# Optimization experiments

Hardware: AMD Instinct MI355X
Metric: run time of the kernel (lower is better)

The kernel has to match this reference:

```python
import jax, jax.numpy as jnp
import numpy as np

BETA = 0.25
K = 1024   # num_codebook_vectors
D = 256    # latent_dim


def setup_inputs() -> dict:
    key = jax.random.key(0)
    k1, k2 = jax.random.split(key)
    z = jax.random.normal(k1, (16, D, 64, 64), dtype=jnp.float32)
    # embedding initialized uniform(-1/K, 1/K) as in the torch module
    emb = jax.random.uniform(k2, (K, D), dtype=jnp.float32, minval=-1.0 / K, maxval=1.0 / K)
    return {"z": z, "emb": emb}


def reference(z, emb):
    sg = jax.lax.stop_gradient
    # NCHW -> NHWC
    z_nhwc = jnp.transpose(z, (0, 2, 3, 1))            # [B,H,W,D]
    zf = z_nhwc.reshape(-1, D)                          # [N,D]
    # squared euclidean distances: ||z||^2 + ||e||^2 - 2 z e^T
    d = (jnp.sum(zf * zf, axis=1, keepdims=True)
         + jnp.sum(emb * emb, axis=1)
         - 2.0 * jnp.matmul(zf, emb.T))                 # [N,K]
    min_encoding_indices = jnp.argmin(d, axis=1)        # [N] int
    z_q = emb[min_encoding_indices].reshape(z_nhwc.shape)  # [B,H,W,D]
    # loss exactly as in source (first term is zero in value, faithful)
    loss = (jnp.mean((sg(z_nhwc) - z_nhwc) ** 2)
            + BETA * jnp.mean((z_q - sg(z_nhwc)) ** 2))
    # straight-through estimator
    z_q_st = z_nhwc + sg(z_q - z_nhwc)
    out = jnp.transpose(z_q_st, (0, 3, 1, 2))           # NHWC -> NCHW
    return out, min_encoding_indices, loss
```

## Files before the change

### kernel.cpp

```cpp
#include <hip/hip_runtime.h>

#define DD 256
#define KK 1024
#define HW 4096
#define NROWSZ 65536
#define OUT_Z 16777216
#define OUT_IDX OUT_Z
#define OUT_LOSS (OUT_Z + NROWSZ)

#define MARGIN 4.5e-4f

#define WS_ESQ   0
#define WS_EH    4096
#define WS_HLIST 528384
#define WS_HCNT  790528
#define WS_LSUM  790536
#define WS_EMBT  791552
#define WS_EHP   1840128

typedef _Float16 f16x8 __attribute__((ext_vector_type(8)));
typedef float f32x4 __attribute__((ext_vector_type(4)));
union U16x8 { uint4 u; f16x8 h; };
typedef unsigned long long u64;

static __device__ __forceinline__ u64 umin64(u64 a, u64 b) { return a < b ? a : b; }
static __device__ __forceinline__ unsigned pk16(float a, float b) {
    _Float16 ha = (_Float16)a, hb = (_Float16)b;
    return (unsigned)__builtin_bit_cast(unsigned short, ha)
         | ((unsigned)__builtin_bit_cast(unsigned short, hb) << 16);
}

__global__ void vq_prep(const float* __restrict__ emb, float* __restrict__ esq,
                        uint2* __restrict__ eh2, int* __restrict__ hcnt,
                        double* __restrict__ lsum, float* __restrict__ embT,
                        int use_embT, uint4* __restrict__ ehP, int use_ehp)
{
    const int bid = blockIdx.x;
    const int t = threadIdx.x;
    if (bid == 0 && t == 0) { *hcnt = 0; *lsum = 0.0; }

    if (bid < 4) {
        int k = bid * 256 + t;
        const float* e = emb + (size_t)k * DD;
        float blk[2];
#pragma unroll
        for (int b2 = 0; b2 < 2; ++b2) {
            const float* p = e + b2 * 128;
            float r[8];
#pragma unroll
            for (int j = 0; j < 8; ++j) r[j] = __fmul_rn(p[j], p[j]);
            for (int i = 8; i < 128; i += 8) {
#pragma unroll
                for (int j = 0; j < 8; ++j)
                    r[j] = __fadd_rn(r[j], __fmul_rn(p[i + j], p[i + j]));
            }
            blk[b2] = __fadd_rn(__fadd_rn(__fadd_rn(r[0], r[1]), __fadd_rn(r[2], r[3])),
                                __fadd_rn(__fadd_rn(r[4], r[5]), __fadd_rn(r[6], r[7])));
        }
        esq[k] = __fadd_rn(blk[0], blk[1]);
    } else if (bid < 20) {
        int tid = (bid - 4) * 256 + t;
        const float4* e4 = (const float4*)emb;
#pragma unroll
        for (int i = 0; i < 16; ++i) {
            int idx = i * 4096 + tid;
            float4 v = e4[idx];
            eh2[idx] = make_uint2(pk16(v.x, v.y), pk16(v.z, v.w));
        }
    } else if (bid < 36) {
        if (!use_embT) return;
        int u = bid - 20;
        int k = u * 64 + (t >> 2);
        int c = t & 3;
        const float4* e4 = (const float4*)(emb + (size_t)k * DD);
#pragma unroll
        for (int i = 0; i < 16; ++i) {
            float4 v = e4[c * 16 + i];
            int d = c * 64 + i * 4;
            embT[(size_t)(d + 0) * KK + k] = v.x;
            embT[(size_t)(d + 1) * KK + k] = v.y;
            embT[(size_t)(d + 2) * KK + k] = v.z;
            embT[(size_t)(d + 3) * KK + k] = v.w;
        }
    } else {
        if (!use_ehp) return;
#pragma unroll
        for (int it = 0; it < 8; ++it) {
            int L = ((bid - 36) * 8 + it) * 256 + t;
            int lane = L & 63, ds = (L >> 6) & 7, wcq = (L >> 9) & 1, tt = L >> 10;
            int col = lane & 15, quad = lane >> 4;
            int code = tt * 32 + wcq * 16 + col;
            int d0 = ds * 32 + quad * 8;
            const float* e = emb + (size_t)code * DD + d0;
            float4 a = *(const float4*)e;
            float4 c4 = *(const float4*)(e + 4);
            ehP[L] = make_uint4(pk16(a.x, a.y), pk16(a.z, a.w),
                                pk16(c4.x, c4.y), pk16(c4.z, c4.w));
        }
    }
}

__launch_bounds__(512, 2)
__global__ void vq_score(const float* __restrict__ z, const _Float16* __restrict__ eh,
                         const uint4* __restrict__ ehP, const float* __restrict__ esq,
                         float* __restrict__ out, int* __restrict__ hlist,
                         int* __restrict__ hcnt, int use_ehp)
{
    __shared__ __align__(16) char zh[256 * 512];
    __shared__ float esq_s[1024];
    __shared__ uint2 cand[256][2];

    const int t = threadIdx.x;
    const int lane = t & 63;
    const int w = t >> 6;
    const int col = lane & 15;
    const int quad = lane >> 4;
    const int wr = w >> 1;
    const int wc = w & 1;

    const int n0 = blockIdx.x * 256;
    const int b = n0 >> 12;
    const int hw0 = n0 & (HW - 1);

    {
        const float* zb2 = z + (size_t)b * DD * HW + hw0;
#pragma unroll 4
        for (int i = 0; i < 32; ++i) {
            const int d = w * 32 + i;
            float4 v = *(const float4*)(zb2 + (size_t)d * HW + lane * 4);
            float va[4] = {v.x, v.y, v.z, v.w};
#pragma unroll
            for (int c = 0; c < 4; ++c) {
                const int row = lane * 4 + c;
                *(_Float16*)(zh + (size_t)row * 512 + ((d * 2) ^ ((row & 7) << 4)))
                    = (_Float16)va[c];
            }
        }
        esq_s[t] = esq[t];
        esq_s[512 + t] = esq[512 + t];
    }
    __syncthreads();

    U16x8 af[4][8];
#pragma unroll
    for (int nt = 0; nt < 4; ++nt) {
        const int row = wr * 64 + nt * 16 + col;
        const int sw = (row & 7) << 4;
#pragma unroll
        for (int ds = 0; ds < 8; ++ds)
            af[nt][ds].u = *(const uint4*)(zh + (size_t)row * 512
                                           + ((ds * 64 + quad * 16) ^ sw));
    }

    unsigned t1[16], t2[16];
#pragma unroll
    for (int i = 0; i < 16; ++i) { t1[i] = 0xFFFFFFFFu; t2[i] = 0xFFFFFFFFu; }

    if (use_ehp) {
        const uint4* bp = ehP + (size_t)wc * 512 + lane;
#pragma unroll 2
        for (int tt = 0; tt < 32; ++tt) {
            const uint4* p = bp + (size_t)tt * 1024;
            U16x8 bf[8];
#pragma unroll
            for (int ds = 0; ds < 8; ++ds) bf[ds].u = p[ds * 64];
            const int code = tt * 32 + wc * 16 + col;
            const float eq1 = 1.0f + esq_s[code];
            f32x4 acc[4];
#pragma unroll
            for (int nt = 0; nt < 4; ++nt) acc[nt] = (f32x4)0.0f;
#pragma unroll
            for (int ds = 0; ds < 8; ++ds)
#pragma unroll
                for (int nt = 0; nt < 4; ++nt)
                    acc[nt] = __builtin_amdgcn_mfma_f32_16x16x32_f16(af[nt][ds].h, bf[ds].h,
                                                                     acc[nt], 0, 0, 0);
#pragma unroll
            for (int nt = 0; nt < 4; ++nt)
#pragma unroll
                for (int r = 0; r < 4; ++r) {
                    float s = fmaf(-2.0f, acc[nt][r], eq1);
                    unsigned k = (__float_as_uint(s) & 0xFFFFFC00u) | (unsigned)code;
                    int mi = nt * 4 + r;
                    t2[mi] = min(t2[mi], max(t1[mi], k));
                    t1[mi] = min(t1[mi], k);
                }
        }
    } else {
        const uint4* ehq = (const uint4*)eh;
        for (int tt = 0; tt < 32; ++tt) {
            const int code = tt * 32 + wc * 16 + col;
            const uint4* bp = ehq + (size_t)code * 32 + quad;
            U16x8 bf[8];
#pragma unroll
            for (int ds = 0; ds < 8; ++ds) bf[ds].u = bp[ds * 4];
            const float eq1 = 1.0f + esq_s[code];
            f32x4 acc[4];
#pragma unroll
            for (int nt = 0; nt < 4; ++nt) acc[nt] = (f32x4)0.0f;
#pragma unroll
            for (int ds = 0; ds < 8; ++ds)
#pragma unroll
                for (int nt = 0; nt < 4; ++nt)
                    acc[nt] = __builtin_amdgcn_mfma_f32_16x16x32_f16(af[nt][ds].h, bf[ds].h,
                                                                     acc[nt], 0, 0, 0);
#pragma unroll
            for (int nt = 0; nt < 4; ++nt)
#pragma unroll
                for (int r = 0; r < 4; ++r) {
                    float s = fmaf(-2.0f, acc[nt][r], eq1);
                    unsigned k = (__float_as_uint(s) & 0xFFFFFC00u) | (unsigned)code;
                    int mi = nt * 4 + r;
                    t2[mi] = min(t2[mi], max(t1[mi], k));
                    t1[mi] = min(t1[mi], k);
                }
        }
    }

#pragma unroll
    for (int mi = 0; mi < 16; ++mi) {
        unsigned a = t1[mi], bb = t2[mi];
#pragma unroll
        for (int off = 1; off < 16; off <<= 1) {
            unsigned o1 = __shfl_xor(a, off, 16);
            unsigned o2 = __shfl_xor(bb, off, 16);
            unsigned mx = max(a, o1);
            a = min(a, o1);
            bb = min(min(bb, o2), mx);
        }
        if (col == 0)
            cand[wr * 64 + (mi >> 2) * 16 + quad * 4 + (mi & 3)][wc] = make_uint2(a, bb);
    }
    __syncthreads();

    if (t < 256) {
        uint2 c0 = cand[t][0], c1 = cand[t][1];
        unsigned mx = max(c0.x, c1.x);
        unsigned a = min(c0.x, c1.x);
        unsigned bb = min(min(c0.y, c1.y), mx);
        float s1 = __uint_as_float(a & 0xFFFFFC00u);
        float s2 = __uint_as_float(bb & 0xFFFFFC00u);
        int k1 = (int)(a & 1023u);
        if (__fsub_rn(s2, s1) > MARGIN) {
            out[OUT_IDX + n0 + t] = (float)k1;
        } else {
            int pos = atomicAdd(hcnt, 1);
            hlist[pos] = n0 + t;
        }
    }
}

template<int USET>
static __device__ __forceinline__ void dot_codes(const float4* __restrict__ embT4,
                                                 const float4* __restrict__ emb4,
                                                 const float4* __restrict__ zb4,
                                                 int t, float (&acc_)[8][4])
{
#pragma unroll 2
    for (int dc = 0; dc < 64; ++dc) {
        float4 e0, e1, e2, e3;
        if (USET) {
            e0 = embT4[(size_t)(dc * 4 + 0) * 256 + t];
            e1 = embT4[(size_t)(dc * 4 + 1) * 256 + t];
            e2 = embT4[(size_t)(dc * 4 + 2) * 256 + t];
            e3 = embT4[(size_t)(dc * 4 + 3) * 256 + t];
        } else {
            float4 a0 = emb4[(size_t)(4 * t + 0) * 64 + dc];
            float4 a1 = emb4[(size_t)(4 * t + 1) * 64 + dc];
            float4 a2 = emb4[(size_t)(4 * t + 2) * 64 + dc];
            float4 a3 = emb4[(size_t)(4 * t + 3) * 64 + dc];
            e0 = make_float4(a0.x, a1.x, a2.x, a3.x);
            e1 = make_float4(a0.y, a1.y, a2.y, a3.y);
            e2 = make_float4(a0.z, a1.z, a2.z, a3.z);
            e3 = make_float4(a0.w, a1.w, a2.w, a3.w);
        }
#pragma unroll
        for (int j = 0; j < 8; ++j) {
            float4 zv = zb4[j * 64 + dc];
            acc_[j][0] = fmaf(zv.x, e0.x, acc_[j][0]);
            acc_[j][1] = fmaf(zv.x, e0.y, acc_[j][1]);
            acc_[j][2] = fmaf(zv.x, e0.z, acc_[j][2]);
            acc_[j][3] = fmaf(zv.x, e0.w, acc_[j][3]);
            acc_[j][0] = fmaf(zv.y, e1.x, acc_[j][0]);
            acc_[j][1] = fmaf(zv.y, e1.y, acc_[j][1]);
            acc_[j][2] = fmaf(zv.y, e1.z, acc_[j][2]);
            acc_[j][3] = fmaf(zv.y, e1.w, acc_[j][3]);
            acc_[j][0] = fmaf(zv.z, e2.x, acc_[j][0]);
            acc_[j][1] = fmaf(zv.z, e2.y, acc_[j][1]);
            acc_[j][2] = fmaf(zv.z, e2.z, acc_[j][2]);
            acc_[j][3] = fmaf(zv.z, e2.w, acc_[j][3]);
            acc_[j][0] = fmaf(zv.w, e3.x, acc_[j][0]);
            acc_[j][1] = fmaf(zv.w, e3.y, acc_[j][1]);
            acc_[j][2] = fmaf(zv.w, e3.z, acc_[j][2]);
            acc_[j][3] = fmaf(zv.w, e3.w, acc_[j][3]);
        }
    }
}

__launch_bounds__(256)
__global__ void vq_hard(const float* __restrict__ z, const float* __restrict__ emb,
                        const float* __restrict__ embT, const float* __restrict__ esq,
                        const int* __restrict__ hlist, const int* __restrict__ hcnt,
                        float* __restrict__ out, int use_embT)
{
    __shared__ __align__(16) float zbuf[8 * 256];
    __shared__ float chains[8][16];
    __shared__ float zq_s[8];
    __shared__ int rows_s[8];
    __shared__ u64 red[4][8];

    const int t = threadIdx.x;
    const int lane = t & 63;
    const int w = t >> 6;
    const int count = *hcnt;

    const float4* embT4 = (const float4*)embT;
    const float4* emb4 = (const float4*)emb;
    const float4* zb4 = (const float4*)zbuf;
    const float4 eqv4 = ((const float4*)esq)[t];
    const float eqa[4] = {eqv4.x, eqv4.y, eqv4.z, eqv4.w};

    for (int g = blockIdx.x; g * 8 < count; g += gridDim.x) {
        __syncthreads();
        if (t < 8) {
            int p = g * 8 + t;
            rows_s[t] = (p < count) ? hlist[p] : -1;
        }
        __syncthreads();

        {
            const int j = t >> 5, dpos = t & 31;
            const int r = rows_s[j];
            float4 v0 = make_float4(0.f, 0.f, 0.f, 0.f), v1 = v0;
            if (r >= 0) {
                const float* zp = z + (size_t)(r >> 12) * (DD * HW) + (r & (HW - 1));
                const int d0 = dpos * 8;
                v0.x = zp[(size_t)(d0 + 0) * HW];
                v0.y = zp[(size_t)(d0 + 1) * HW];
                v0.z = zp[(size_t)(d0 + 2) * HW];
                v0.w = zp[(size_t)(d0 + 3) * HW];
                v1.x = zp[(size_t)(d0 + 4) * HW];
                v1.y = zp[(size_t)(d0 + 5) * HW];
                v1.z = zp[(size_t)(d0 + 6) * HW];
                v1.w = zp[(size_t)(d0 + 7) * HW];
            }
            *(float4*)&zbuf[j * 256 + dpos * 8] = v0;
            *(float4*)&zbuf[j * 256 + dpos * 8 + 4] = v1;
        }
        __syncthreads();

        if (t < 128) {
            int j = t >> 4, c = t & 15, b2 = c >> 3, jj = c & 7;
            const float* p = &zbuf[j * 256];
            int base = b2 * 128 + jj;
            float v = p[base];
            float acc = __fmul_rn(v, v);
            for (int i = 1; i < 16; ++i) {
                float u = p[base + i * 8];
                acc = __fadd_rn(acc, __fmul_rn(u, u));
            }
            chains[j][c] = acc;
        }
        __syncthreads();
        if (t < 8) {
            const float* c = chains[t];
            float b0 = __fadd_rn(__fadd_rn(__fadd_rn(c[0], c[1]), __fadd_rn(c[2], c[3])),
                                 __fadd_rn(__fadd_rn(c[4], c[5]), __fadd_rn(c[6], c[7])));
            float b1 = __fadd_rn(__fadd_rn(__fadd_rn(c[8], c[9]), __fadd_rn(c[10], c[11])),
                                 __fadd_rn(__fadd_rn(c[12], c[13]), __fadd_rn(c[14], c[15])));
            zq_s[t] = __fadd_rn(b0, b1);
        }
        __syncthreads();

        float acc_[8][4];
#pragma unroll
        for (int j = 0; j < 8; ++j)
#pragma unroll
            for (int kk = 0; kk < 4; ++kk) acc_[j][kk] = 0.0f;

        if (use_embT) dot_codes<1>(embT4, emb4, zb4, t, acc_);
        else          dot_codes<0>(embT4, emb4, zb4, t, acc_);

#pragma unroll
        for (int j = 0; j < 8; ++j) {
            u64 m = ~0ull;
#pragma unroll
            for (int kk = 0; kk < 4; ++kk) {
                float s = __fsub_rn(__fadd_rn(zq_s[j], eqa[kk]),
                                    __fmul_rn(2.0f, acc_[j][kk]));
                u64 p = ((u64)__float_as_uint(s) << 32) | (unsigned)(4 * t + kk);
                m = umin64(m, p);
            }
#pragma unroll
            for (int off = 1; off < 64; off <<= 1)
                m = umin64(m, __shfl_xor(m, off, 64));
            if (lane == 0) red[w][j] = m;
        }
        __syncthreads();
        if (t < 8) {
            u64 m = umin64(umin64(red[0][t], red[1][t]), umin64(red[2][t], red[3][t]));
            int r = rows_s[t];
            if (r >= 0) out[OUT_IDX + r] = (float)(int)(m & 0xffffffffu);
        }
    }
}

__launch_bounds__(256)
__global__ void vq_out(const float* __restrict__ z, const float* __restrict__ emb,
                       const float* __restrict__ embT, float* out,
                       double* __restrict__ lsum, int use_embT)
{
    __shared__ float et[8 * 1024];
    __shared__ float wsum[4];

    const int t = threadIdx.x;
    const int lane = t & 63;
    const int w = t >> 6;
    const int bb = blockIdx.x >> 5;
    const int dg = blockIdx.x & 31;

    if (use_embT) {
#pragma unroll
        for (int c = 0; c < 8; ++c)
            *(float4*)&et[c * 1024 + t * 4] =
                *(const float4*)&embT[(size_t)(dg * 8 + c) * KK + t * 4];
    } else {
        for (int i = 0; i < 32; ++i) {
            int kk = i * 256 + t;
            et[kk] = emb[(size_t)(kk & 1023) * DD + dg * 8 + (kk >> 10)];
        }
    }
    __syncthreads();

    float lacc = 0.f;
    const size_t zb = (size_t)bb * DD * HW;
    const float* idxf = out + OUT_IDX + (size_t)bb * HW;
#pragma unroll
    for (int ch = 0; ch < 4; ++ch) {
        const int hw = ch * 1024 + t * 4;
        float4 fi = *(const float4*)&idxf[hw];
        int k0 = (int)fi.x, k1 = (int)fi.y, k2 = (int)fi.z, k3 = (int)fi.w;
#pragma unroll
        for (int dl = 0; dl < 8; ++dl) {
            size_t off = zb + (size_t)(dg * 8 + dl) * HW + hw;
            float4 zv = *(const float4*)&z[off];
            float4 e;
            e.x = et[dl * 1024 + k0];
            e.y = et[dl * 1024 + k1];
            e.z = et[dl * 1024 + k2];
            e.w = et[dl * 1024 + k3];
            *(float4*)&out[off] = e;
            float df;
            df = e.x - zv.x; lacc = fmaf(df, df, lacc);
            df = e.y - zv.y; lacc = fmaf(df, df, lacc);
            df = e.z - zv.z; lacc = fmaf(df, df, lacc);
            df = e.w - zv.w; lacc = fmaf(df, df, lacc);
        }
    }
#pragma unroll
    for (int off = 32; off > 0; off >>= 1) lacc += __shfl_down(lacc, off, 64);
    if (lane == 0) wsum[w] = lacc;
    __syncthreads();
    if (t == 0) {
        double tot = (double)wsum[0] + (double)wsum[1] + (double)wsum[2] + (double)wsum[3];
        atomicAdd(lsum, tot);
    }
}

__global__ void vq_final(const double* __restrict__ lsum, float* __restrict__ out)
{
    out[OUT_LOSS] = (float)(0.25 * (lsum[0] / (double)OUT_Z));
}

extern "C" void kernel_launch(void* const* d_in, const int* in_sizes, int n_in,
                              void* d_out, int out_size, void* d_ws, size_t ws_size,
                              hipStream_t stream)
{
    const float* z = (const float*)d_in[0];
    const float* emb = (const float*)d_in[1];
    float* out = (float*)d_out;
    char* w = (char*)d_ws;

    float* esq = (float*)(w + WS_ESQ);
    _Float16* eh = (_Float16*)(w + WS_EH);
    uint2* eh2 = (uint2*)(w + WS_EH);
    int* hlist = (int*)(w + WS_HLIST);
    int* hcnt = (int*)(w + WS_HCNT);
    double* lsum = (double*)(w + WS_LSUM);
    float* embT = (float*)(w + WS_EMBT);
    uint4* ehP = (uint4*)(w + WS_EHP);

    int use_embT = (ws_size >= (size_t)WS_EMBT + (size_t)DD * KK * sizeof(float)) ? 1 : 0;
    int use_ehp = (ws_size >= (size_t)WS_EHP + (size_t)KK * DD * sizeof(_Float16)) ? 1 : 0;

    vq_prep<<<dim3(52), dim3(256), 0, stream>>>(emb, esq, eh2, hcnt, lsum, embT, use_embT,
                                                ehP, use_ehp);
    vq_score<<<dim3(256), dim3(512), 0, stream>>>(z, eh, ehP, esq, out, hlist, hcnt,
                                                  use_ehp);
    vq_hard<<<dim3(1024), dim3(256), 0, stream>>>(z, emb, embT, esq, hlist, hcnt, out,
                                                  use_embT);
    vq_out<<<dim3(512), dim3(256), 0, stream>>>(z, emb, embT, out, lsum, use_embT);
    vq_final<<<dim3(1), dim3(1), 0, stream>>>(lsum, out);
}
```

Measured before the change: 245.0 us.

## Repartition score kernel so each wave owns 32 rows across all codes

After: 247.4 us. About the same (+1.0%).

```diff
diff --git a/kernel.cpp b/kernel.cpp
--- a/kernel.cpp
+++ b/kernel.cpp
@@ -87,9 +87,9 @@
 #pragma unroll
         for (int it = 0; it < 8; ++it) {
             int L = ((bid - 36) * 8 + it) * 256 + t;
-            int lane = L & 63, ds = (L >> 6) & 7, wcq = (L >> 9) & 1, tt = L >> 10;
+            int lane = L & 63, ds = (L >> 6) & 7, t16 = L >> 9;
             int col = lane & 15, quad = lane >> 4;
-            int code = tt * 32 + wcq * 16 + col;
+            int code = t16 * 16 + col;
             int d0 = ds * 32 + quad * 8;
             const float* e = emb + (size_t)code * DD + d0;
             float4 a = *(const float4*)e;
@@ -108,43 +108,45 @@
 {
     __shared__ __align__(16) char zh[256 * 512];
     __shared__ float esq_s[1024];
-    __shared__ uint2 cand[256][2];
+    __shared__ uint2 cand[256];
 
     const int t = threadIdx.x;
     const int lane = t & 63;
     const int w = t >> 6;
     const int col = lane & 15;
     const int quad = lane >> 4;
-    const int wr = w >> 1;
-    const int wc = w & 1;
 
     const int n0 = blockIdx.x * 256;
     const int b = n0 >> 12;
     const int hw0 = n0 & (HW - 1);
 
     {
-        const float* zb2 = z + (size_t)b * DD * HW + hw0;
-#pragma unroll 4
-        for (int i = 0; i < 32; ++i) {
-            const int d = w * 32 + i;
-            float4 v = *(const float4*)(zb2 + (size_t)d * HW + lane * 4);
-            float va[4] = {v.x, v.y, v.z, v.w};
-#pragma unroll
-            for (int c = 0; c < 4; ++c) {
-                const int row = lane * 4 + c;
-                *(_Float16*)(zh + (size_t)row * 512 + ((d * 2) ^ ((row & 7) << 4)))
-                    = (_Float16)va[c];
-            }
+        const int row = t & 255;
+        const int dh = t >> 8;
+        const float* src = z + (size_t)b * DD * HW + hw0 + row;
+#pragma unroll
+        for (int i = 0; i < 16; ++i) {
+            const int d0 = dh * 128 + i * 8;
+            float v0 = src[(size_t)(d0 + 0) * HW];
+            float v1 = src[(size_t)(d0 + 1) * HW];
+            float v2 = src[(size_t)(d0 + 2) * HW];
+            float v3 = src[(size_t)(d0 + 3) * HW];
+            float v4 = src[(size_t)(d0 + 4) * HW];
+            float v5 = src[(size_t)(d0 + 5) * HW];
+            float v6 = src[(size_t)(d0 + 6) * HW];
+            float v7 = src[(size_t)(d0 + 7) * HW];
+            uint4 pk = make_uint4(pk16(v0, v1), pk16(v2, v3), pk16(v4, v5), pk16(v6, v7));
+            *(uint4*)(zh + (size_t)row * 512 + ((d0 * 2) ^ ((row & 7) << 4))) = pk;
         }
         esq_s[t] = esq[t];
         esq_s[512 + t] = esq[512 + t];
     }
     __syncthreads();
 
-    U16x8 af[4][8];
-#pragma unroll
-    for (int nt = 0; nt < 4; ++nt) {
-        const int row = wr * 64 + nt * 16 + col;
+    U16x8 af[2][8];
+#pragma unroll
+    for (int nt = 0; nt < 2; ++nt) {
+        const int row = w * 32 + nt * 16 + col;
         const int sw = (row & 7) << 4;
 #pragma unroll
         for (int ds = 0; ds < 8; ++ds)
@@ -152,73 +154,63 @@
                                            + ((ds * 64 + quad * 16) ^ sw));
     }
 
-    unsigned t1[16], t2[16];
-#pragma unroll
-    for (int i = 0; i < 16; ++i) { t1[i] = 0xFFFFFFFFu; t2[i] = 0xFFFFFFFFu; }
+    unsigned t1[8], t2[8];
+#pragma unroll
+    for (int i = 0; i < 8; ++i) { t1[i] = 0xFFFFFFFFu; t2[i] = 0xFFFFFFFFu; }
+
+    auto proc = [&](U16x8 (&bf)[8], int t16) {
+        const int code = t16 * 16 + col;
+        const float eq1 = 1.0f + esq_s[code];
+        f32x4 acc0 = (f32x4)0.0f, acc1 = (f32x4)0.0f;
+#pragma unroll
+        for (int ds = 0; ds < 8; ++ds) {
+            acc0 = __builtin_amdgcn_mfma_f32_16x16x32_f16(af[0][ds].h, bf[ds].h, acc0, 0, 0, 0);
+            acc1 = __builtin_amdgcn_mfma_f32_16x16x32_f16(af[1][ds].h, bf[ds].h, acc1, 0, 0, 0);
+        }
+#pragma unroll
+        for (int r = 0; r < 4; ++r) {
+            float s0 = fmaf(-2.0f, acc0[r], eq1);
+            unsigned k0 = (__float_as_uint(s0) & 0xFFFFFC00u) | (unsigned)code;
+            t2[r] = min(t2[r], max(t1[r], k0));
+            t1[r] = min(t1[r], k0);
+            float s1 = fmaf(-2.0f, acc1[r], eq1);
+            unsigned k1 = (__float_as_uint(s1) & 0xFFFFFC00u) | (unsigned)code;
+            t2[4 + r] = min(t2[4 + r], max(t1[4 + r], k1));
+            t1[4 + r] = min(t1[4 + r], k1);
+        }
+    };
 
     if (use_ehp) {
-        const uint4* bp = ehP + (size_t)wc * 512 + lane;
-#pragma unroll 2
-        for (int tt = 0; tt < 32; ++tt) {
-            const uint4* p = bp + (size_t)tt * 1024;
-            U16x8 bf[8];
-#pragma unroll
-            for (int ds = 0; ds < 8; ++ds) bf[ds].u = p[ds * 64];
-            const int code = tt * 32 + wc * 16 + col;
-            const float eq1 = 1.0f + esq_s[code];
-            f32x4 acc[4];
-#pragma unroll
-            for (int nt = 0; nt < 4; ++nt) acc[nt] = (f32x4)0.0f;
-#pragma unroll
-            for (int ds = 0; ds < 8; ++ds)
-#pragma unroll
-                for (int nt = 0; nt < 4; ++nt)
-                    acc[nt] = __builtin_amdgcn_mfma_f32_16x16x32_f16(af[nt][ds].h, bf[ds].h,
-                                                                     acc[nt], 0, 0, 0);
-#pragma unroll
-            for (int nt = 0; nt < 4; ++nt)
-#pragma unroll
-                for (int r = 0; r < 4; ++r) {
-                    float s = fmaf(-2.0f, acc[nt][r], eq1);
-                    unsigned k = (__float_as_uint(s) & 0xFFFFFC00u) | (unsigned)code;
-                    int mi = nt * 4 + r;
-                    t2[mi] = min(t2[mi], max(t1[mi], k));
-                    t1[mi] = min(t1[mi], k);
-                }
+        const uint4* bq = ehP + lane;
+        U16x8 bfA[8], bfB[8];
+#pragma unroll
+        for (int ds = 0; ds < 8; ++ds) bfA[ds].u = bq[ds * 64];
+#pragma unroll 1
+        for (int t16 = 0; t16 < 64; t16 += 2) {
+            const uint4* p1 = bq + (size_t)(t16 + 1) * 512;
+#pragma unroll
+            for (int ds = 0; ds < 8; ++ds) bfB[ds].u = p1[ds * 64];
+            proc(bfA, t16);
+            const uint4* p2 = bq + (size_t)((t16 + 2) & 63) * 512;
+#pragma unroll
+            for (int ds = 0; ds < 8; ++ds) bfA[ds].u = p2[ds * 64];
+            proc(bfB, t16 + 1);
+            if ((t16 & 6) == 6) __builtin_amdgcn_s_barrier();
         }
     } else {
         const uint4* ehq = (const uint4*)eh;
-        for (int tt = 0; tt < 32; ++tt) {
-            const int code = tt * 32 + wc * 16 + col;
-            const uint4* bp = ehq + (size_t)code * 32 + quad;
+#pragma unroll 1
+        for (int t16 = 0; t16 < 64; ++t16) {
+            const uint4* bp = ehq + (size_t)(t16 * 16 + col) * 32 + quad;
             U16x8 bf[8];
 #pragma unroll
             for (int ds = 0; ds < 8; ++ds) bf[ds].u = bp[ds * 4];
-            const float eq1 = 1.0f + esq_s[code];
-            f32x4 acc[4];
-#pragma unroll
-            for (int nt = 0; nt < 4; ++nt) acc[nt] = (f32x4)0.0f;
-#pragma unroll
-            for (int ds = 0; ds < 8; ++ds)
-#pragma unroll
-                for (int nt = 0; nt < 4; ++nt)
-                    acc[nt] = __builtin_amdgcn_mfma_f32_16x16x32_f16(af[nt][ds].h, bf[ds].h,
-                                                                     acc[nt], 0, 0, 0);
-#pragma unroll
-            for (int nt = 0; nt < 4; ++nt)
-#pragma unroll
-                for (int r = 0; r < 4; ++r) {
-                    float s = fmaf(-2.0f, acc[nt][r], eq1);
-                    unsigned k = (__float_as_uint(s) & 0xFFFFFC00u) | (unsigned)code;
-                    int mi = nt * 4 + r;
-                    t2[mi] = min(t2[mi], max(t1[mi], k));
-                    t1[mi] = min(t1[mi], k);
-                }
-        }
-    }
-
-#pragma unroll
-    for (int mi = 0; mi < 16; ++mi) {
+            proc(bf, t16);
+        }
+    }
+
+#pragma unroll
+    for (int mi = 0; mi < 8; ++mi) {
         unsigned a = t1[mi], bb = t2[mi];
 #pragma unroll
         for (int off = 1; off < 16; off <<= 1) {
@@ -229,18 +221,15 @@
             bb = min(min(bb, o2), mx);
         }
         if (col == 0)
-            cand[wr * 64 + (mi >> 2) * 16 + quad * 4 + (mi & 3)][wc] = make_uint2(a, bb);
+            cand[w * 32 + (mi >> 2) * 16 + quad * 4 + (mi & 3)] = make_uint2(a, bb);
     }
     __syncthreads();
 
     if (t < 256) {
-        uint2 c0 = cand[t][0], c1 = cand[t][1];
-        unsigned mx = max(c0.x, c1.x);
-        unsigned a = min(c0.x, c1.x);
-        unsigned bb = min(min(c0.y, c1.y), mx);
-        float s1 = __uint_as_float(a & 0xFFFFFC00u);
-        float s2 = __uint_as_float(bb & 0xFFFFFC00u);
-        int k1 = (int)(a & 1023u);
+        uint2 c = cand[t];
+        float s1 = __uint_as_float(c.x & 0xFFFFFC00u);
+        float s2 = __uint_as_float(c.y & 0xFFFFFC00u);
+        int k1 = (int)(c.x & 1023u);
         if (__fsub_rn(s2, s1) > MARGIN) {
             out[OUT_IDX + n0 + t] = (float)k1;
         } else {
```
